# Performance work log

Hardware: AMD Instinct MI355X
Metric: run time of the kernel (lower is better)

## Reference

```python
import jax, jax.numpy as jnp
import numpy as np

TEMPERATURE = 8.0  # sqrt(head_dim=64)
NEG = -1e9


def setup_inputs() -> dict:
    key = jax.random.key(0)
    kq, kk, kv = jax.random.split(key, 3)
    B, H, S, D = 2, 16, 2048, 64
    q = jax.random.normal(kq, (B, H, S, D), dtype=jnp.float32)
    k = jax.random.normal(kk, (B, H, S, D), dtype=jnp.float32)
    v = jax.random.normal(kv, (B, H, S, D), dtype=jnp.float32)
    attn_mask = jnp.ones((B, 1, 1, S), dtype=jnp.int32)  # 1 = keep, 0 = mask
    return {"q": q, "k": k, "v": v, "attn_mask": attn_mask}


def reference(q, k, v, attn_mask):
    # attn = (q / T) @ k^T  -> [B,H,S,S]
    scores = jnp.einsum('bhqd,bhkd->bhqk', q / TEMPERATURE, k)
    # optional padding mask: fill where mask == 0
    scores = jnp.where(attn_mask == 0, NEG, scores)
    # causal mask: triu(diagonal=1) positions are masked (key index > query index)
    S = scores.shape[-1]
    row = jnp.arange(S)[:, None]
    col = jnp.arange(S)[None, :]
    scores = jnp.where(col > row, NEG, scores)
    attn = jax.nn.softmax(scores, axis=-1)
    out = jnp.einsum('bhqk,bhkd->bhqd', attn, v)
    return (out, attn)
```

## Files before the change

kernel.cpp:

```cpp
#include <hip/hip_runtime.h>

#define NEG (-1e9f)

typedef __attribute__((ext_vector_type(8))) short bf16x8;
typedef __attribute__((ext_vector_type(4))) float f32x4;

static constexpr int Ss = 2048, Dd = 64;

__device__ __forceinline__ unsigned short f2bf(float f) {
  union { float f; unsigned u; } v; v.f = f;
  unsigned r = v.u + 0x7FFF + ((v.u >> 16) & 1);
  return (unsigned short)(r >> 16);
}

__device__ __forceinline__ void gl_lds16(const unsigned short* g, unsigned short* l) {
  __builtin_amdgcn_global_load_lds(
      (const __attribute__((address_space(1))) unsigned int*)g,
      (__attribute__((address_space(3))) unsigned int*)l, 16, 0, 0);
}

#define PIDX(row, col) ((((row) * 64) + (col)) ^ (((row) & 7) << 3))

__global__ __launch_bounds__(256) void prep_kernel(
    const float* __restrict__ k, const float* __restrict__ v,
    unsigned short* __restrict__ kbf, unsigned short* __restrict__ vtbf) {
  const int tid = threadIdx.x;
  const int bh = blockIdx.x >> 5;
  const int j  = blockIdx.x & 31;
  __shared__ __align__(16) unsigned short Kl[64 * 72];
  __shared__ __align__(16) unsigned short Vl[64 * 72];
  const size_t base = ((size_t)bh * Ss + (size_t)j * 64) * Dd;
#pragma unroll
  for (int i = 0; i < 4; ++i) {
    int idx4 = tid + i * 256;
    int row = idx4 >> 4, col = (idx4 & 15) * 4;
    float4 f = *(const float4*)(k + base + row * 64 + col);
    ushort4 u;
    u.x = f2bf(f.x); u.y = f2bf(f.y); u.z = f2bf(f.z); u.w = f2bf(f.w);
    *(ushort4*)&Kl[row * 72 + col] = u;
    float4 g = *(const float4*)(v + base + row * 64 + col);
    ushort4 w;
    w.x = f2bf(g.x); w.y = f2bf(g.y); w.z = f2bf(g.z); w.w = f2bf(g.w);
    *(ushort4*)&Vl[row * 72 + col] = w;
  }
  __syncthreads();
  const size_t tb = ((size_t)bh * 32 + j) * 4096;
#pragma unroll
  for (int t = 0; t < 2; ++t) {
    int id = tid + t * 256;
    int ck = id >> 6, ln = id & 63;
    int c = ck >> 1, ph = ck & 1;
    bf16x8 val = *(const bf16x8*)&Kl[(c * 16 + (ln & 15)) * 72 + (ln >> 4) * 8 + ph * 32];
    *(bf16x8*)&kbf[tb + ck * 512 + ln * 8] = val;
  }
#pragma unroll
  for (int t = 0; t < 2; ++t) {
    int id = tid + t * 256;
    int ck = id >> 6, ln = id & 63;
    int c = ck >> 1, ch = ck & 1;
    bf16x8 val;
#pragma unroll
    for (int i = 0; i < 8; ++i)
      val[i] = (short)Vl[(ch * 32 + (ln >> 4) * 8 + i) * 72 + c * 16 + (ln & 15)];
    *(bf16x8*)&vtbf[tb + ck * 512 + ln * 8] = val;
  }
}

__global__ __launch_bounds__(256) void attn_kernel(
    const float* __restrict__ q, const unsigned short* __restrict__ kbf,
    const unsigned short* __restrict__ vtbf, const int* __restrict__ mask,
    float* __restrict__ out, float* __restrict__ attn) {
  const int tid = threadIdx.x;
  const int wave = tid >> 6, lane = tid & 63, quad = lane >> 4, ln15 = lane & 15;
  const int bh = blockIdx.x & 31;
  const int g = blockIdx.x >> 5, h = g & 7, kk = g >> 3;
  const int qt = (kk < 2) ? (h * 2 + kk) : (31 - h * 2 - (kk & 1));
  const int b = bh >> 4;
  const int qloc = wave * 16 + ln15;
  const int qg = qt * 64 + qloc;

  __shared__ __align__(16) unsigned short Kb[2 * 4096];
  __shared__ __align__(16) unsigned short Vb[2 * 4096];
  __shared__ __align__(16) unsigned short Plds[4096];

  bf16x8 qf0, qf1;
  {
    const float* qp = q + ((size_t)bh * Ss + qg) * Dd + quad * 8;
    float4 f0 = *(const float4*)(qp);
    float4 f1 = *(const float4*)(qp + 4);
    float4 f2 = *(const float4*)(qp + 32);
    float4 f3 = *(const float4*)(qp + 36);
    qf0[0] = (short)f2bf(f0.x * 0.125f); qf0[1] = (short)f2bf(f0.y * 0.125f);
    qf0[2] = (short)f2bf(f0.z * 0.125f); qf0[3] = (short)f2bf(f0.w * 0.125f);
    qf0[4] = (short)f2bf(f1.x * 0.125f); qf0[5] = (short)f2bf(f1.y * 0.125f);
    qf0[6] = (short)f2bf(f1.z * 0.125f); qf0[7] = (short)f2bf(f1.w * 0.125f);
    qf1[0] = (short)f2bf(f2.x * 0.125f); qf1[1] = (short)f2bf(f2.y * 0.125f);
    qf1[2] = (short)f2bf(f2.z * 0.125f); qf1[3] = (short)f2bf(f2.w * 0.125f);
    qf1[4] = (short)f2bf(f3.x * 0.125f); qf1[5] = (short)f2bf(f3.y * 0.125f);
    qf1[6] = (short)f2bf(f3.z * 0.125f); qf1[7] = (short)f2bf(f3.w * 0.125f);
  }

  const unsigned short* kt = kbf + ((size_t)bh * 32) * 4096;
  const unsigned short* vt = vtbf + ((size_t)bh * 32) * 4096;
  const int* mrowp = mask + (size_t)b * Ss;
  const int c0 = wave * 2, c1 = wave * 2 + 1;

  float m = -1e30f, l = 0.0f;

  gl_lds16(kt + c0 * 512 + lane * 8, &Kb[c0 * 512]);
  gl_lds16(kt + c1 * 512 + lane * 8, &Kb[c1 * 512]);
  __syncthreads();
  for (int j = 0; j <= qt; ++j) {
    const int cur = j & 1;
    if (j < qt) {
      const unsigned short* nt = kt + (size_t)(j + 1) * 4096;
      gl_lds16(nt + c0 * 512 + lane * 8, &Kb[(cur ^ 1) * 4096 + c0 * 512]);
      gl_lds16(nt + c1 * 512 + lane * 8, &Kb[(cur ^ 1) * 4096 + c1 * 512]);
    }
    unsigned long long mm = __ballot(mrowp[j * 64 + lane] != 0);
    float sv[16];
#pragma unroll
    for (int c = 0; c < 4; ++c) {
      bf16x8 kf0 = *(const bf16x8*)&Kb[cur * 4096 + (c * 2 + 0) * 512 + lane * 8];
      bf16x8 kf1 = *(const bf16x8*)&Kb[cur * 4096 + (c * 2 + 1) * 512 + lane * 8];
      f32x4 acc = {0.f, 0.f, 0.f, 0.f};
      acc = __builtin_amdgcn_mfma_f32_16x16x32_bf16(kf0, qf0, acc, 0, 0, 0);
      acc = __builtin_amdgcn_mfma_f32_16x16x32_bf16(kf1, qf1, acc, 0, 0, 0);
#pragma unroll
      for (int r = 0; r < 4; ++r) sv[c * 4 + r] = acc[r];
    }
    if (j == qt || mm != ~0ull) {
#pragma unroll
      for (int c = 0; c < 4; ++c)
#pragma unroll
        for (int r = 0; r < 4; ++r) {
          int kl = c * 16 + quad * 4 + r;
          bool mz = !((mm >> kl) & 1);
          if (j * 64 + kl > qg || mz) sv[c * 4 + r] = NEG;
        }
    }
    float t0 = fmaxf(fmaxf(sv[0], sv[1]), fmaxf(sv[2], sv[3]));
    float t1 = fmaxf(fmaxf(sv[4], sv[5]), fmaxf(sv[6], sv[7]));
    float t2 = fmaxf(fmaxf(sv[8], sv[9]), fmaxf(sv[10], sv[11]));
    float t3 = fmaxf(fmaxf(sv[12], sv[13]), fmaxf(sv[14], sv[15]));
    float tm = fmaxf(fmaxf(t0, t1), fmaxf(t2, t3));
    tm = fmaxf(tm, __shfl_xor(tm, 16));
    tm = fmaxf(tm, __shfl_xor(tm, 32));
    float mnew = fmaxf(m, tm);
    float ss = 0.f;
#pragma unroll
    for (int i = 0; i < 16; ++i) ss += __expf(sv[i] - mnew);
    ss += __shfl_xor(ss, 16);
    ss += __shfl_xor(ss, 32);
    l = l * __expf(m - mnew) + ss;
    m = mnew;
    __syncthreads();
  }

  const float rl = 1.0f / l;
  f32x4 oacc[4];
#pragma unroll
  for (int c = 0; c < 4; ++c) oacc[c] = (f32x4){0.f, 0.f, 0.f, 0.f};
  float* arow = attn + ((size_t)bh * Ss + qg) * Ss;

  gl_lds16(kt + c0 * 512 + lane * 8, &Kb[c0 * 512]);
  gl_lds16(kt + c1 * 512 + lane * 8, &Kb[c1 * 512]);
  gl_lds16(vt + c0 * 512 + lane * 8, &Vb[c0 * 512]);
  gl_lds16(vt + c1 * 512 + lane * 8, &Vb[c1 * 512]);
  __syncthreads();
  for (int j = 0; j <= qt; ++j) {
    const int cur = j & 1;
    if (j < qt) {
      const unsigned short* ntk = kt + (size_t)(j + 1) * 4096;
      const unsigned short* ntv = vt + (size_t)(j + 1) * 4096;
      gl_lds16(ntk + c0 * 512 + lane * 8, &Kb[(cur ^ 1) * 4096 + c0 * 512]);
      gl_lds16(ntk + c1 * 512 + lane * 8, &Kb[(cur ^ 1) * 4096 + c1 * 512]);
      gl_lds16(ntv + c0 * 512 + lane * 8, &Vb[(cur ^ 1) * 4096 + c0 * 512]);
      gl_lds16(ntv + c1 * 512 + lane * 8, &Vb[(cur ^ 1) * 4096 + c1 * 512]);
    }
    unsigned long long mm = __ballot(mrowp[j * 64 + lane] != 0);
    float sv[16];
#pragma unroll
    for (int c = 0; c < 4; ++c) {
      bf16x8 kf0 = *(const bf16x8*)&Kb[cur * 4096 + (c * 2 + 0) * 512 + lane * 8];
      bf16x8 kf1 = *(const bf16x8*)&Kb[cur * 4096 + (c * 2 + 1) * 512 + lane * 8];
      f32x4 acc = {0.f, 0.f, 0.f, 0.f};
      acc = __builtin_amdgcn_mfma_f32_16x16x32_bf16(kf0, qf0, acc, 0, 0, 0);
      acc = __builtin_amdgcn_mfma_f32_16x16x32_bf16(kf1, qf1, acc, 0, 0, 0);
#pragma unroll
      for (int r = 0; r < 4; ++r) sv[c * 4 + r] = acc[r];
    }
    if (j == qt || mm != ~0ull) {
#pragma unroll
      for (int c = 0; c < 4; ++c)
#pragma unroll
        for (int r = 0; r < 4; ++r) {
          int kl = c * 16 + quad * 4 + r;
          bool mz = !((mm >> kl) & 1);
          if (j * 64 + kl > qg || mz) sv[c * 4 + r] = NEG;
        }
    }
#pragma unroll
    for (int c = 0; c < 4; ++c) {
      float4 pv;
      pv.x = __expf(sv[c * 4 + 0] - m) * rl;
      pv.y = __expf(sv[c * 4 + 1] - m) * rl;
      pv.z = __expf(sv[c * 4 + 2] - m) * rl;
      pv.w = __expf(sv[c * 4 + 3] - m) * rl;
      *(float4*)&arow[j * 64 + c * 16 + quad * 4] = pv;
      ushort4 u;
      u.x = f2bf(pv.x); u.y = f2bf(pv.y); u.z = f2bf(pv.z); u.w = f2bf(pv.w);
      *(ushort4*)&Plds[PIDX(qloc, c * 16 + quad * 4)] = u;
    }
#pragma unroll
    for (int ch = 0; ch < 2; ++ch) {
      bf16x8 pf = *(const bf16x8*)&Plds[PIDX(qloc, quad * 8 + 32 * ch)];
#pragma unroll
      for (int c = 0; c < 4; ++c) {
        bf16x8 vf = *(const bf16x8*)&Vb[cur * 4096 + (c * 2 + ch) * 512 + lane * 8];
        oacc[c] = __builtin_amdgcn_mfma_f32_16x16x32_bf16(vf, pf, oacc[c], 0, 0, 0);
      }
    }
    __syncthreads();
  }

  for (int j = qt + 1; j < 32; ++j) {
    float4 z = {0.f, 0.f, 0.f, 0.f};
#pragma unroll
    for (int i = 0; i < 4; ++i) {
      int idx4 = tid + i * 256;
      int row = idx4 >> 4, col = (idx4 & 15) * 4;
      *(float4*)&attn[((size_t)bh * Ss + qt * 64 + row) * Ss + j * 64 + col] = z;
    }
  }

#pragma unroll
  for (int c = 0; c < 4; ++c)
    *(f32x4*)&out[((size_t)bh * Ss + qg) * Dd + c * 16 + quad * 4] = oacc[c];
}

__global__ __launch_bounds__(256) void attn_kernel_fb(
    const float* __restrict__ q, const float* __restrict__ k,
    const float* __restrict__ v, const int* __restrict__ mask,
    float* __restrict__ out, float* __restrict__ attn) {
  const int tid  = threadIdx.x;
  const int wave = tid >> 6;
  const int lane = tid & 63;
  const int quad = lane >> 4;
  const int ln15 = lane & 15;

  const int bh = blockIdx.x & 31;
  const int qt = 31 - (blockIdx.x >> 5);
  const int b  = bh >> 4;

  __shared__ unsigned short Klds[64 * 72];
  __shared__ unsigned short Vlds[64 * 72];
  __shared__ unsigned short Plds2[64 * 72];

  {
    const float* qp = q + ((size_t)bh * Ss + (size_t)qt * 64) * Dd;
#pragma unroll
    for (int i = 0; i < 4; ++i) {
      int idx4 = tid + i * 256;
      int row = idx4 >> 4, col = (idx4 & 15) * 4;
      float4 f = *(const float4*)(qp + row * 64 + col);
      ushort4 u;
      u.x = f2bf(f.x * 0.125f); u.y = f2bf(f.y * 0.125f);
      u.z = f2bf(f.z * 0.125f); u.w = f2bf(f.w * 0.125f);
      *(ushort4*)&Vlds[row * 72 + col] = u;
    }
  }
  __syncthreads();
  const bf16x8 qfrag0 = *(const bf16x8*)&Vlds[(wave * 16 + ln15) * 72 + quad * 8];
  const bf16x8 qfrag1 = *(const bf16x8*)&Vlds[(wave * 16 + ln15) * 72 + quad * 8 + 32];

  float mrow[4], lrow[4];
#pragma unroll
  for (int r = 0; r < 4; ++r) { mrow[r] = -1e30f; lrow[r] = 0.0f; }

  for (int j = 0; j <= qt; ++j) {
    __syncthreads();
    {
      const float* kp = k + ((size_t)bh * Ss + (size_t)j * 64) * Dd;
#pragma unroll
      for (int i = 0; i < 4; ++i) {
        int idx4 = tid + i * 256;
        int row = idx4 >> 4, col = (idx4 & 15) * 4;
        float4 f = *(const float4*)(kp + row * 64 + col);
        ushort4 u;
        u.x = f2bf(f.x); u.y = f2bf(f.y); u.z = f2bf(f.z); u.w = f2bf(f.w);
        *(ushort4*)&Klds[row * 72 + col] = u;
      }
    }
    __syncthreads();
    unsigned long long mm = __ballot(mask[(size_t)b * Ss + j * 64 + lane] != 0);

    float sv[4][4];
#pragma unroll
    for (int c = 0; c < 4; ++c) {
      bf16x8 kf0 = *(const bf16x8*)&Klds[(c * 16 + ln15) * 72 + quad * 8];
      bf16x8 kf1 = *(const bf16x8*)&Klds[(c * 16 + ln15) * 72 + quad * 8 + 32];
      f32x4 acc = {0.f, 0.f, 0.f, 0.f};
      acc = __builtin_amdgcn_mfma_f32_16x16x32_bf16(qfrag0, kf0, acc, 0, 0, 0);
      acc = __builtin_amdgcn_mfma_f32_16x16x32_bf16(qfrag1, kf1, acc, 0, 0, 0);
      int col = j * 64 + c * 16 + ln15;
      bool mz = !((mm >> (c * 16 + ln15)) & 1);
#pragma unroll
      for (int r = 0; r < 4; ++r) {
        int row = qt * 64 + wave * 16 + quad * 4 + r;
        float val = acc[r];
        if (col > row || mz) val = NEG;
        sv[c][r] = val;
      }
    }
#pragma unroll
    for (int r = 0; r < 4; ++r) {
      float tm = fmaxf(fmaxf(sv[0][r], sv[1][r]), fmaxf(sv[2][r], sv[3][r]));
      tm = fmaxf(tm, __shfl_xor(tm, 1));
      tm = fmaxf(tm, __shfl_xor(tm, 2));
      tm = fmaxf(tm, __shfl_xor(tm, 4));
      tm = fmaxf(tm, __shfl_xor(tm, 8));
      float mnew = fmaxf(mrow[r], tm);
      float ss = __expf(sv[0][r] - mnew) + __expf(sv[1][r] - mnew) +
                 __expf(sv[2][r] - mnew) + __expf(sv[3][r] - mnew);
      ss += __shfl_xor(ss, 1);
      ss += __shfl_xor(ss, 2);
      ss += __shfl_xor(ss, 4);
      ss += __shfl_xor(ss, 8);
      lrow[r] = lrow[r] * __expf(mrow[r] - mnew) + ss;
      mrow[r] = mnew;
    }
  }

  float rl4[4];
#pragma unroll
  for (int r = 0; r < 4; ++r) rl4[r] = 1.0f / lrow[r];

  f32x4 oacc[4];
#pragma unroll
  for (int c = 0; c < 4; ++c) oacc[c] = (f32x4){0.f, 0.f, 0.f, 0.f};

  for (int j = 0; j < 32; ++j) {
    if (j <= qt) {
      __syncthreads();
      {
        const float* kp = k + ((size_t)bh * Ss + (size_t)j * 64) * Dd;
        const float* vp = v + ((size_t)bh * Ss + (size_t)j * 64) * Dd;
#pragma unroll
        for (int i = 0; i < 4; ++i) {
          int idx4 = tid + i * 256;
          int row = idx4 >> 4, col = (idx4 & 15) * 4;
          float4 f = *(const float4*)(kp + row * 64 + col);
          ushort4 u;
          u.x = f2bf(f.x); u.y = f2bf(f.y); u.z = f2bf(f.z); u.w = f2bf(f.w);
          *(ushort4*)&Klds[row * 72 + col] = u;
          float4 g = *(const float4*)(vp + row * 64 + col);
          ushort4 w2;
          w2.x = f2bf(g.x); w2.y = f2bf(g.y); w2.z = f2bf(g.z); w2.w = f2bf(g.w);
          *(ushort4*)&Vlds[row * 72 + col] = w2;
        }
      }
      __syncthreads();
      unsigned long long mm = __ballot(mask[(size_t)b * Ss + j * 64 + lane] != 0);
#pragma unroll
      for (int c = 0; c < 4; ++c) {
        bf16x8 kf0 = *(const bf16x8*)&Klds[(c * 16 + ln15) * 72 + quad * 8];
        bf16x8 kf1 = *(const bf16x8*)&Klds[(c * 16 + ln15) * 72 + quad * 8 + 32];
        f32x4 acc = {0.f, 0.f, 0.f, 0.f};
        acc = __builtin_amdgcn_mfma_f32_16x16x32_bf16(qfrag0, kf0, acc, 0, 0, 0);
        acc = __builtin_amdgcn_mfma_f32_16x16x32_bf16(qfrag1, kf1, acc, 0, 0, 0);
        int col = j * 64 + c * 16 + ln15;
        bool mz = !((mm >> (c * 16 + ln15)) & 1);
#pragma unroll
        for (int r = 0; r < 4; ++r) {
          int row = qt * 64 + wave * 16 + quad * 4 + r;
          float val = acc[r];
          if (col > row || mz) val = NEG;
          float p = __expf(val - mrow[r]) * rl4[r];
          attn[((size_t)bh * Ss + row) * Ss + col] = p;
          Plds2[(wave * 16 + quad * 4 + r) * 72 + c * 16 + ln15] = f2bf(p);
        }
      }
#pragma unroll
      for (int ch = 0; ch < 2; ++ch) {
        bf16x8 pf = *(const bf16x8*)&Plds2[(wave * 16 + ln15) * 72 + quad * 8 + 32 * ch];
#pragma unroll
        for (int c = 0; c < 4; ++c) {
          bf16x8 vf;
#pragma unroll
          for (int jj = 0; jj < 8; ++jj)
            vf[jj] = (short)Vlds[(quad * 8 + jj + 32 * ch) * 72 + c * 16 + ln15];
          oacc[c] = __builtin_amdgcn_mfma_f32_16x16x32_bf16(pf, vf, oacc[c], 0, 0, 0);
        }
      }
    } else {
      float4 z = {0.f, 0.f, 0.f, 0.f};
#pragma unroll
      for (int i = 0; i < 4; ++i) {
        int idx4 = tid + i * 256;
        int row = idx4 >> 4, col = (idx4 & 15) * 4;
        *(float4*)&attn[((size_t)bh * Ss + qt * 64 + row) * Ss + j * 64 + col] = z;
      }
    }
  }

#pragma unroll
  for (int c = 0; c < 4; ++c)
#pragma unroll
    for (int r = 0; r < 4; ++r) {
      int row = qt * 64 + wave * 16 + quad * 4 + r;
      out[((size_t)bh * Ss + row) * Dd + c * 16 + ln15] = oacc[c][r];
    }
}

extern "C" void kernel_launch(void* const* d_in, const int* in_sizes, int n_in,
                              void* d_out, int out_size, void* d_ws, size_t ws_size,
                              hipStream_t stream) {
  const float* q    = (const float*)d_in[0];
  const float* k    = (const float*)d_in[1];
  const float* v    = (const float*)d_in[2];
  const int*   mask = (const int*)d_in[3];
  float* out  = (float*)d_out;
  float* attn = out + (size_t)2 * 16 * 2048 * 64;

  const size_t need = (size_t)2 * 32 * Ss * Dd * sizeof(unsigned short);
  if (d_ws != nullptr && ws_size >= need) {
    unsigned short* kbf  = (unsigned short*)d_ws;
    unsigned short* vtbf = kbf + (size_t)32 * Ss * Dd;
    prep_kernel<<<dim3(32 * 32), dim3(256), 0, stream>>>(k, v, kbf, vtbf);
    attn_kernel<<<dim3(32 * 32), dim3(256), 0, stream>>>(q, kbf, vtbf, mask, out, attn);
  } else {
    attn_kernel_fb<<<dim3(32 * 32), dim3(256), 0, stream>>>(q, k, v, mask, out, attn);
  }
}
```

Baseline: 646.7 us.

## Use Cauchy-Schwarz bound as fixed softmax shift and deepen K prefetch pipeline

The prep kernel now records, per batch-head, the maximum squared key norm, and sets a global flag if any padding-mask entry is zero. The fast attention kernel uses sqrt(|q|^2 * max|k|^2) as a fixed softmax shift. This removes the running max, the rescaling and the per-tile mask ballot from the first pass, and turns the second pass into a single exp per element. A separate fallback launch handles inputs whose mask is not all ones. The first pass also moves to a 4-deep K prefetch ring with explicit vmcnt waits and raw barriers. The cost is an extra init launch, a fallback launch that always runs even when it exits at once, and a risk of exp underflow when the bound sits far above the true row maximum.

```diff
diff --git a/kernel.cpp b/kernel.cpp
--- a/kernel.cpp
+++ b/kernel.cpp
@@ -21,14 +21,22 @@
 
 #define PIDX(row, col) ((((row) * 64) + (col)) ^ (((row) & 7) << 3))
 
+__global__ void init_kernel(unsigned* flagsM) {
+  if (threadIdx.x < 64) flagsM[threadIdx.x] = 0;
+}
+
 __global__ __launch_bounds__(256) void prep_kernel(
     const float* __restrict__ k, const float* __restrict__ v,
-    unsigned short* __restrict__ kbf, unsigned short* __restrict__ vtbf) {
+    const int* __restrict__ mask,
+    unsigned short* __restrict__ kbf, unsigned short* __restrict__ vtbf,
+    unsigned* __restrict__ flagsM) {
   const int tid = threadIdx.x;
   const int bh = blockIdx.x >> 5;
   const int j  = blockIdx.x & 31;
+  const int b  = bh >> 4;
   __shared__ __align__(16) unsigned short Kl[64 * 72];
   __shared__ __align__(16) unsigned short Vl[64 * 72];
+  __shared__ float pn[64][16];
   const size_t base = ((size_t)bh * Ss + (size_t)j * 64) * Dd;
 #pragma unroll
   for (int i = 0; i < 4; ++i) {
@@ -38,6 +46,7 @@
     ushort4 u;
     u.x = f2bf(f.x); u.y = f2bf(f.y); u.z = f2bf(f.z); u.w = f2bf(f.w);
     *(ushort4*)&Kl[row * 72 + col] = u;
+    pn[row][idx4 & 15] = f.x * f.x + f.y * f.y + f.z * f.z + f.w * f.w;
     float4 g = *(const float4*)(v + base + row * 64 + col);
     ushort4 w;
     w.x = f2bf(g.x); w.y = f2bf(g.y); w.z = f2bf(g.z); w.w = f2bf(g.w);
@@ -64,149 +73,170 @@
       val[i] = (short)Vl[(ch * 32 + (ln >> 4) * 8 + i) * 72 + c * 16 + (ln & 15)];
     *(bf16x8*)&vtbf[tb + ck * 512 + ln * 8] = val;
   }
-}
-
-__global__ __launch_bounds__(256) void attn_kernel(
+  if (tid < 64) {
+    const float4* pr = (const float4*)pn[tid];
+    float4 a = pr[0], bq = pr[1], cq = pr[2], dq = pr[3];
+    float s = a.x + a.y + a.z + a.w + bq.x + bq.y + bq.z + bq.w +
+              cq.x + cq.y + cq.z + cq.w + dq.x + dq.y + dq.z + dq.w;
+#pragma unroll
+    for (int x = 1; x <= 32; x <<= 1) s = fmaxf(s, __shfl_xor(s, x));
+    if (tid == 0) atomicMax(&flagsM[1 + bh], __float_as_uint(s));
+  } else if (tid < 128) {
+    int lane = tid - 64;
+    unsigned long long mm = __ballot(mask[(size_t)b * Ss + j * 64 + lane] == 0);
+    if (lane == 0 && mm != 0ull) atomicOr(&flagsM[0], 1u);
+  }
+}
+
+__global__ __launch_bounds__(256) void attn_fast(
     const float* __restrict__ q, const unsigned short* __restrict__ kbf,
-    const unsigned short* __restrict__ vtbf, const int* __restrict__ mask,
+    const unsigned short* __restrict__ vtbf, const unsigned* __restrict__ flagsM,
     float* __restrict__ out, float* __restrict__ attn) {
+  if (flagsM[0] != 0) return;
   const int tid = threadIdx.x;
   const int wave = tid >> 6, lane = tid & 63, quad = lane >> 4, ln15 = lane & 15;
   const int bh = blockIdx.x & 31;
-  const int g = blockIdx.x >> 5, h = g & 7, kk = g >> 3;
-  const int qt = (kk < 2) ? (h * 2 + kk) : (31 - h * 2 - (kk & 1));
-  const int b = bh >> 4;
+  const int g = blockIdx.x >> 5, h = g & 7, kk2 = g >> 3;
+  const int qt = (kk2 < 2) ? (h * 2 + kk2) : (31 - h * 2 - (kk2 & 1));
   const int qloc = wave * 16 + ln15;
   const int qg = qt * 64 + qloc;
 
-  __shared__ __align__(16) unsigned short Kb[2 * 4096];
-  __shared__ __align__(16) unsigned short Vb[2 * 4096];
+  __shared__ __align__(16) unsigned short S4[4 * 4096];
   __shared__ __align__(16) unsigned short Plds[4096];
 
   bf16x8 qf0, qf1;
+  float qn2;
   {
     const float* qp = q + ((size_t)bh * Ss + qg) * Dd + quad * 8;
     float4 f0 = *(const float4*)(qp);
     float4 f1 = *(const float4*)(qp + 4);
     float4 f2 = *(const float4*)(qp + 32);
     float4 f3 = *(const float4*)(qp + 36);
-    qf0[0] = (short)f2bf(f0.x * 0.125f); qf0[1] = (short)f2bf(f0.y * 0.125f);
-    qf0[2] = (short)f2bf(f0.z * 0.125f); qf0[3] = (short)f2bf(f0.w * 0.125f);
-    qf0[4] = (short)f2bf(f1.x * 0.125f); qf0[5] = (short)f2bf(f1.y * 0.125f);
-    qf0[6] = (short)f2bf(f1.z * 0.125f); qf0[7] = (short)f2bf(f1.w * 0.125f);
-    qf1[0] = (short)f2bf(f2.x * 0.125f); qf1[1] = (short)f2bf(f2.y * 0.125f);
-    qf1[2] = (short)f2bf(f2.z * 0.125f); qf1[3] = (short)f2bf(f2.w * 0.125f);
-    qf1[4] = (short)f2bf(f3.x * 0.125f); qf1[5] = (short)f2bf(f3.y * 0.125f);
-    qf1[6] = (short)f2bf(f3.z * 0.125f); qf1[7] = (short)f2bf(f3.w * 0.125f);
-  }
+    float s0 = f0.x * 0.125f, s1 = f0.y * 0.125f, s2 = f0.z * 0.125f, s3 = f0.w * 0.125f;
+    float s4 = f1.x * 0.125f, s5 = f1.y * 0.125f, s6 = f1.z * 0.125f, s7 = f1.w * 0.125f;
+    float t0 = f2.x * 0.125f, t1 = f2.y * 0.125f, t2 = f2.z * 0.125f, t3 = f2.w * 0.125f;
+    float t4 = f3.x * 0.125f, t5 = f3.y * 0.125f, t6 = f3.z * 0.125f, t7 = f3.w * 0.125f;
+    qf0[0] = (short)f2bf(s0); qf0[1] = (short)f2bf(s1); qf0[2] = (short)f2bf(s2); qf0[3] = (short)f2bf(s3);
+    qf0[4] = (short)f2bf(s4); qf0[5] = (short)f2bf(s5); qf0[6] = (short)f2bf(s6); qf0[7] = (short)f2bf(s7);
+    qf1[0] = (short)f2bf(t0); qf1[1] = (short)f2bf(t1); qf1[2] = (short)f2bf(t2); qf1[3] = (short)f2bf(t3);
+    qf1[4] = (short)f2bf(t4); qf1[5] = (short)f2bf(t5); qf1[6] = (short)f2bf(t6); qf1[7] = (short)f2bf(t7);
+    qn2 = s0*s0 + s1*s1 + s2*s2 + s3*s3 + s4*s4 + s5*s5 + s6*s6 + s7*s7 +
+          t0*t0 + t1*t1 + t2*t2 + t3*t3 + t4*t4 + t5*t5 + t6*t6 + t7*t7;
+    qn2 += __shfl_xor(qn2, 16);
+    qn2 += __shfl_xor(qn2, 32);
+  }
+  const float Mn2 = __uint_as_float(flagsM[1 + bh]);
+  const float C = sqrtf(qn2 * Mn2);
 
   const unsigned short* kt = kbf + ((size_t)bh * 32) * 4096;
   const unsigned short* vt = vtbf + ((size_t)bh * 32) * 4096;
-  const int* mrowp = mask + (size_t)b * Ss;
-  const int c0 = wave * 2, c1 = wave * 2 + 1;
-
-  float m = -1e30f, l = 0.0f;
-
-  gl_lds16(kt + c0 * 512 + lane * 8, &Kb[c0 * 512]);
-  gl_lds16(kt + c1 * 512 + lane * 8, &Kb[c1 * 512]);
-  __syncthreads();
+  const int c0 = wave * 2, c1 = c0 + 1;
+
+  asm volatile("s_waitcnt vmcnt(0)" ::: "memory");
+
+#pragma unroll
+  for (int t = 0; t < 3; ++t) {
+    const unsigned short* src = kt + (size_t)((t <= qt) ? t : qt) * 4096;
+    gl_lds16(src + c0 * 512 + lane * 8, &S4[t * 4096 + c0 * 512]);
+    gl_lds16(src + c1 * 512 + lane * 8, &S4[t * 4096 + c1 * 512]);
+  }
+  float l0 = 0.f, l1 = 0.f, l2 = 0.f, l3 = 0.f;
   for (int j = 0; j <= qt; ++j) {
-    const int cur = j & 1;
-    if (j < qt) {
-      const unsigned short* nt = kt + (size_t)(j + 1) * 4096;
-      gl_lds16(nt + c0 * 512 + lane * 8, &Kb[(cur ^ 1) * 4096 + c0 * 512]);
-      gl_lds16(nt + c1 * 512 + lane * 8, &Kb[(cur ^ 1) * 4096 + c1 * 512]);
-    }
-    unsigned long long mm = __ballot(mrowp[j * 64 + lane] != 0);
+    asm volatile("s_waitcnt vmcnt(4)" ::: "memory");
+    __builtin_amdgcn_s_barrier();
+    asm volatile("" ::: "memory");
+    {
+      int nt = (j + 3 <= qt) ? (j + 3) : qt;
+      const unsigned short* src = kt + (size_t)nt * 4096;
+      unsigned short* dst = &S4[((j + 3) & 3) * 4096];
+      gl_lds16(src + c0 * 512 + lane * 8, dst + c0 * 512);
+      gl_lds16(src + c1 * 512 + lane * 8, dst + c1 * 512);
+    }
+    asm volatile("" ::: "memory");
+    const unsigned short* sl = &S4[(j & 3) * 4096];
     float sv[16];
 #pragma unroll
     for (int c = 0; c < 4; ++c) {
-      bf16x8 kf0 = *(const bf16x8*)&Kb[cur * 4096 + (c * 2 + 0) * 512 + lane * 8];
-      bf16x8 kf1 = *(const bf16x8*)&Kb[cur * 4096 + (c * 2 + 1) * 512 + lane * 8];
+      bf16x8 kf0 = *(const bf16x8*)&sl[(c * 2 + 0) * 512 + lane * 8];
+      bf16x8 kf1 = *(const bf16x8*)&sl[(c * 2 + 1) * 512 + lane * 8];
       f32x4 acc = {0.f, 0.f, 0.f, 0.f};
       acc = __builtin_amdgcn_mfma_f32_16x16x32_bf16(kf0, qf0, acc, 0, 0, 0);
       acc = __builtin_amdgcn_mfma_f32_16x16x32_bf16(kf1, qf1, acc, 0, 0, 0);
 #pragma unroll
       for (int r = 0; r < 4; ++r) sv[c * 4 + r] = acc[r];
     }
-    if (j == qt || mm != ~0ull) {
+    if (j == qt) {
 #pragma unroll
       for (int c = 0; c < 4; ++c)
 #pragma unroll
-        for (int r = 0; r < 4; ++r) {
-          int kl = c * 16 + quad * 4 + r;
-          bool mz = !((mm >> kl) & 1);
-          if (j * 64 + kl > qg || mz) sv[c * 4 + r] = NEG;
-        }
-    }
-    float t0 = fmaxf(fmaxf(sv[0], sv[1]), fmaxf(sv[2], sv[3]));
-    float t1 = fmaxf(fmaxf(sv[4], sv[5]), fmaxf(sv[6], sv[7]));
-    float t2 = fmaxf(fmaxf(sv[8], sv[9]), fmaxf(sv[10], sv[11]));
-    float t3 = fmaxf(fmaxf(sv[12], sv[13]), fmaxf(sv[14], sv[15]));
-    float tm = fmaxf(fmaxf(t0, t1), fmaxf(t2, t3));
-    tm = fmaxf(tm, __shfl_xor(tm, 16));
-    tm = fmaxf(tm, __shfl_xor(tm, 32));
-    float mnew = fmaxf(m, tm);
-    float ss = 0.f;
-#pragma unroll
-    for (int i = 0; i < 16; ++i) ss += __expf(sv[i] - mnew);
-    ss += __shfl_xor(ss, 16);
-    ss += __shfl_xor(ss, 32);
-    l = l * __expf(m - mnew) + ss;
-    m = mnew;
-    __syncthreads();
-  }
-
-  const float rl = 1.0f / l;
+        for (int r = 0; r < 4; ++r)
+          if (c * 16 + quad * 4 + r > qloc) sv[c * 4 + r] = NEG;
+    }
+#pragma unroll
+    for (int i = 0; i < 16; i += 4) {
+      l0 += __expf(sv[i + 0] - C);
+      l1 += __expf(sv[i + 1] - C);
+      l2 += __expf(sv[i + 2] - C);
+      l3 += __expf(sv[i + 3] - C);
+    }
+  }
+  float l = (l0 + l1) + (l2 + l3);
+  l += __shfl_xor(l, 16);
+  l += __shfl_xor(l, 32);
+  const float msum = C + __logf(l);
+
+  __syncthreads();
+
   f32x4 oacc[4];
 #pragma unroll
   for (int c = 0; c < 4; ++c) oacc[c] = (f32x4){0.f, 0.f, 0.f, 0.f};
   float* arow = attn + ((size_t)bh * Ss + qg) * Ss;
 
-  gl_lds16(kt + c0 * 512 + lane * 8, &Kb[c0 * 512]);
-  gl_lds16(kt + c1 * 512 + lane * 8, &Kb[c1 * 512]);
-  gl_lds16(vt + c0 * 512 + lane * 8, &Vb[c0 * 512]);
-  gl_lds16(vt + c1 * 512 + lane * 8, &Vb[c1 * 512]);
-  __syncthreads();
+  gl_lds16(kt + c0 * 512 + lane * 8, &S4[c0 * 512]);
+  gl_lds16(kt + c1 * 512 + lane * 8, &S4[c1 * 512]);
+  gl_lds16(vt + c0 * 512 + lane * 8, &S4[4096 + c0 * 512]);
+  gl_lds16(vt + c1 * 512 + lane * 8, &S4[4096 + c1 * 512]);
+  asm volatile("s_waitcnt vmcnt(0)" ::: "memory");
+  __builtin_amdgcn_s_barrier();
+  asm volatile("" ::: "memory");
   for (int j = 0; j <= qt; ++j) {
-    const int cur = j & 1;
+    const unsigned short* Ksl = &S4[(j & 1) * 8192];
+    const unsigned short* Vsl = Ksl + 4096;
     if (j < qt) {
       const unsigned short* ntk = kt + (size_t)(j + 1) * 4096;
       const unsigned short* ntv = vt + (size_t)(j + 1) * 4096;
-      gl_lds16(ntk + c0 * 512 + lane * 8, &Kb[(cur ^ 1) * 4096 + c0 * 512]);
-      gl_lds16(ntk + c1 * 512 + lane * 8, &Kb[(cur ^ 1) * 4096 + c1 * 512]);
-      gl_lds16(ntv + c0 * 512 + lane * 8, &Vb[(cur ^ 1) * 4096 + c0 * 512]);
-      gl_lds16(ntv + c1 * 512 + lane * 8, &Vb[(cur ^ 1) * 4096 + c1 * 512]);
-    }
-    unsigned long long mm = __ballot(mrowp[j * 64 + lane] != 0);
+      unsigned short* d = &S4[((j + 1) & 1) * 8192];
+      gl_lds16(ntk + c0 * 512 + lane * 8, d + c0 * 512);
+      gl_lds16(ntk + c1 * 512 + lane * 8, d + c1 * 512);
+      gl_lds16(ntv + c0 * 512 + lane * 8, d + 4096 + c0 * 512);
+      gl_lds16(ntv + c1 * 512 + lane * 8, d + 4096 + c1 * 512);
+    }
+    asm volatile("" ::: "memory");
     float sv[16];
 #pragma unroll
     for (int c = 0; c < 4; ++c) {
-      bf16x8 kf0 = *(const bf16x8*)&Kb[cur * 4096 + (c * 2 + 0) * 512 + lane * 8];
-      bf16x8 kf1 = *(const bf16x8*)&Kb[cur * 4096 + (c * 2 + 1) * 512 + lane * 8];
+      bf16x8 kf0 = *(const bf16x8*)&Ksl[(c * 2 + 0) * 512 + lane * 8];
+      bf16x8 kf1 = *(const bf16x8*)&Ksl[(c * 2 + 1) * 512 + lane * 8];
       f32x4 acc = {0.f, 0.f, 0.f, 0.f};
       acc = __builtin_amdgcn_mfma_f32_16x16x32_bf16(kf0, qf0, acc, 0, 0, 0);
       acc = __builtin_amdgcn_mfma_f32_16x16x32_bf16(kf1, qf1, acc, 0, 0, 0);
 #pragma unroll
       for (int r = 0; r < 4; ++r) sv[c * 4 + r] = acc[r];
     }
-    if (j == qt || mm != ~0ull) {
+    if (j == qt) {
 #pragma unroll
       for (int c = 0; c < 4; ++c)
 #pragma unroll
-        for (int r = 0; r < 4; ++r) {
-          int kl = c * 16 + quad * 4 + r;
-          bool mz = !((mm >> kl) & 1);
-          if (j * 64 + kl > qg || mz) sv[c * 4 + r] = NEG;
-        }
+        for (int r = 0; r < 4; ++r)
+          if (c * 16 + quad * 4 + r > qloc) sv[c * 4 + r] = NEG;
     }
 #pragma unroll
     for (int c = 0; c < 4; ++c) {
       float4 pv;
-      pv.x = __expf(sv[c * 4 + 0] - m) * rl;
-      pv.y = __expf(sv[c * 4 + 1] - m) * rl;
-      pv.z = __expf(sv[c * 4 + 2] - m) * rl;
-      pv.w = __expf(sv[c * 4 + 3] - m) * rl;
+      pv.x = __expf(sv[c * 4 + 0] - msum);
+      pv.y = __expf(sv[c * 4 + 1] - msum);
+      pv.z = __expf(sv[c * 4 + 2] - msum);
+      pv.w = __expf(sv[c * 4 + 3] - msum);
       *(float4*)&arow[j * 64 + c * 16 + quad * 4] = pv;
       ushort4 u;
       u.x = f2bf(pv.x); u.y = f2bf(pv.y); u.z = f2bf(pv.z); u.w = f2bf(pv.w);
@@ -217,11 +247,13 @@
       bf16x8 pf = *(const bf16x8*)&Plds[PIDX(qloc, quad * 8 + 32 * ch)];
 #pragma unroll
       for (int c = 0; c < 4; ++c) {
-        bf16x8 vf = *(const bf16x8*)&Vb[cur * 4096 + (c * 2 + ch) * 512 + lane * 8];
+        bf16x8 vf = *(const bf16x8*)&Vsl[(c * 2 + ch) * 512 + lane * 8];
         oacc[c] = __builtin_amdgcn_mfma_f32_16x16x32_bf16(vf, pf, oacc[c], 0, 0, 0);
       }
     }
-    __syncthreads();
+    asm volatile("s_waitcnt vmcnt(4)" ::: "memory");
+    __builtin_amdgcn_s_barrier();
+    asm volatile("" ::: "memory");
   }
 
   for (int j = qt + 1; j < 32; ++j) {
@@ -242,7 +274,9 @@
 __global__ __launch_bounds__(256) void attn_kernel_fb(
     const float* __restrict__ q, const float* __restrict__ k,
     const float* __restrict__ v, const int* __restrict__ mask,
-    float* __restrict__ out, float* __restrict__ attn) {
+    float* __restrict__ out, float* __restrict__ attn,
+    const unsigned* __restrict__ flagsM, int force) {
+  if (!force && flagsM[0] == 0) return;
   const int tid  = threadIdx.x;
   const int wave = tid >> 6;
   const int lane = tid & 63;
@@ -354,9 +388,9 @@
           ushort4 u;
           u.x = f2bf(f.x); u.y = f2bf(f.y); u.z = f2bf(f.z); u.w = f2bf(f.w);
           *(ushort4*)&Klds[row * 72 + col] = u;
-          float4 g = *(const float4*)(vp + row * 64 + col);
+          float4 gg = *(const float4*)(vp + row * 64 + col);
           ushort4 w2;
-          w2.x = f2bf(g.x); w2.y = f2bf(g.y); w2.z = f2bf(g.z); w2.w = f2bf(g.w);
+          w2.x = f2bf(gg.x); w2.y = f2bf(gg.y); w2.z = f2bf(gg.z); w2.w = f2bf(gg.w);
           *(ushort4*)&Vlds[row * 72 + col] = w2;
         }
       }
@@ -423,13 +457,16 @@
   float* out  = (float*)d_out;
   float* attn = out + (size_t)2 * 16 * 2048 * 64;
 
-  const size_t need = (size_t)2 * 32 * Ss * Dd * sizeof(unsigned short);
+  const size_t need = 256 + (size_t)2 * 32 * Ss * Dd * sizeof(unsigned short);
   if (d_ws != nullptr && ws_size >= need) {
-    unsigned short* kbf  = (unsigned short*)d_ws;
+    unsigned* flagsM = (unsigned*)d_ws;
+    unsigned short* kbf  = (unsigned short*)((char*)d_ws + 256);
     unsigned short* vtbf = kbf + (size_t)32 * Ss * Dd;
-    prep_kernel<<<dim3(32 * 32), dim3(256), 0, stream>>>(k, v, kbf, vtbf);
-    attn_kernel<<<dim3(32 * 32), dim3(256), 0, stream>>>(q, kbf, vtbf, mask, out, attn);
+    init_kernel<<<dim3(1), dim3(64), 0, stream>>>(flagsM);
+    prep_kernel<<<dim3(32 * 32), dim3(256), 0, stream>>>(k, v, mask, kbf, vtbf, flagsM);
+    attn_fast<<<dim3(32 * 32), dim3(256), 0, stream>>>(q, kbf, vtbf, flagsM, out, attn);
+    attn_kernel_fb<<<dim3(32 * 32), dim3(256), 0, stream>>>(q, k, v, mask, out, attn, flagsM, 0);
   } else {
-    attn_kernel_fb<<<dim3(32 * 32), dim3(256), 0, stream>>>(q, k, v, mask, out, attn);
-  }
-}
+    attn_kernel_fb<<<dim3(32 * 32), dim3(256), 0, stream>>>(q, k, v, mask, out, attn, nullptr, 1);
+  }
+}
```

After: 633.3 us. 1.02x faster.
